# Kernel tuning notes

Measured on AMD Instinct MI355X. Metric: run time of the kernel, lower is better.

The kernel has to match this reference:

```python
import jax, jax.numpy as jnp
import numpy as np

N_NODES = 10000
N_EDGES = 160000
BN_EPS = 1e-5


def _sage(xx, src, dst, Wl, bl, Wr, n):
    # SAGEConv: lin_l(mean of in-neighbors) + lin_r(x)
    s = jax.ops.segment_sum(xx[src], dst, num_segments=n)
    cnt = jax.ops.segment_sum(jnp.ones((src.shape[0], 1), xx.dtype), dst, num_segments=n)
    mean = s / jnp.maximum(cnt, 1.0)
    return mean @ Wl + bl + xx @ Wr


def _gin(xx, src, dst, W1, b1, W2, b2, n):
    # GINConv (eps=0): MLP(x + sum of neighbors), MLP = Lin-ReLU-Lin-ReLU
    agg = xx + jax.ops.segment_sum(xx[src], dst, num_segments=n)
    h = jax.nn.relu(agg @ W1 + b1)
    return jax.nn.relu(h @ W2 + b2)


def _gat(xx, s2, d2, W, a_s, a_d, b, heads, ch, n):
    # GATConv with self-loops already appended in (s2, d2)
    h = (xx @ W).reshape(n, heads, ch)          # [N,H,C]
    al_s = (h * a_s).sum(-1)                     # [N,H]
    al_d = (h * a_d).sum(-1)                     # [N,H]
    e = jax.nn.leaky_relu(al_s[s2] + al_d[d2], negative_slope=0.2)  # [E',H]
    m = jax.ops.segment_max(e, d2, num_segments=n)
    ex = jnp.exp(e - m[d2])
    den = jax.ops.segment_sum(ex, d2, num_segments=n)
    coef = ex / den[d2]                          # segment softmax over dst
    out = jax.ops.segment_sum(h[s2] * coef[:, :, None], d2, num_segments=n)
    return out.reshape(n, heads * ch) + b


def reference(x, edge_index, train_edge_id,
              Wp1, bp1, Wp2, bp2, Wp3, bp3,
              sage1_Wl, sage1_bl, sage1_Wr, sage2_Wl, sage2_bl, sage2_Wr,
              gin1_W1, gin1_b1, gin1_W2, gin1_b2,
              gin2_W1, gin2_b1, gin2_W2, gin2_b2, gin_lin_W, gin_lin_b,
              gat1_W, gat1_as, gat1_ad, gat1_b,
              gat2_W, gat2_as, gat2_ad, gat2_b,
              fusion_w, lin1_W, lin1_b, lin2_W, lin2_b, fc2_W, fc2_b):
    n = x.shape[0]
    src, dst = edge_index[0], edge_index[1]
    # --- ppc: PointNet-style encoder: per-point MLP (16->64->128->256) + max pool over points ---
    pts = x[:, :, :16]                            # [N,L,16]
    h = jax.nn.relu(pts @ Wp1 + bp1)
    h = jax.nn.relu(h @ Wp2 + bp2)
    h = jax.nn.relu(h @ Wp3 + bp3)
    feat = h.max(axis=1)                          # [N,256]
    # --- SAGE branch ---
    hs = jax.nn.relu(_sage(feat, src, dst, sage1_Wl, sage1_bl, sage1_Wr, n))
    out_sage = _sage(hs, src, dst, sage2_Wl, sage2_bl, sage2_Wr, n)
    # --- GIN branch ---
    hg = jax.nn.relu(_gin(feat, src, dst, gin1_W1, gin1_b1, gin1_W2, gin1_b2, n))
    hg = jax.nn.relu(_gin(hg, src, dst, gin2_W1, gin2_b1, gin2_W2, gin2_b2, n))
    out_gin = hg @ gin_lin_W + gin_lin_b
    # --- GAT branch (self-loops per PyG default) ---
    loop = jnp.arange(n)
    s2 = jnp.concatenate([src, loop])
    d2 = jnp.concatenate([dst, loop])
    ha = jax.nn.relu(_gat(feat, s2, d2, gat1_W, gat1_as, gat1_ad, gat1_b, 8, 10, n))
    out_gat = _gat(ha, s2, d2, gat2_W, gat2_as, gat2_ad, gat2_b, 1, 512, n)
    # --- weighted fusion + batch norm (batch stats, no affine) ---
    y = fusion_w[0] * out_sage + fusion_w[1] * out_gin + fusion_w[2] * out_gat
    mu = y.mean(axis=0)
    var = y.var(axis=0)
    y = (y - mu) / jnp.sqrt(var + BN_EPS)
    # --- head ---
    y = jax.nn.relu(y @ lin1_W + lin1_b)
    y = y @ lin2_W + lin2_b
    # --- edge-pair gather + multiply for link scoring ---
    nid = edge_index[:, train_edge_id]            # [2,T]
    z = y[nid[0]] * y[nid[1]]
    return z @ fc2_W + fc2_b                      # [T,7]


def setup_inputs() -> dict:
    key = jax.random.key(0)
    ks = iter(jax.random.split(key, 64))
    def nrm(shape, s=0.02):
        return jax.random.normal(next(ks), shape, dtype=jnp.float32) * s
    inp = {}
    inp['x'] = jax.random.normal(next(ks), (N_NODES, 128, 16), dtype=jnp.float32)
    inp['edge_index'] = jax.random.randint(next(ks), (2, N_EDGES), 0, N_NODES, dtype=jnp.int32)
    inp['train_edge_id'] = jax.random.randint(next(ks), (50000,), 0, N_EDGES, dtype=jnp.int32)
    # ppc point encoder
    inp['Wp1'] = nrm((16, 64)); inp['bp1'] = nrm((64,))
    inp['Wp2'] = nrm((64, 128)); inp['bp2'] = nrm((128,))
    inp['Wp3'] = nrm((128, 256)); inp['bp3'] = nrm((256,))
    # SAGE: 256->128->512
    inp['sage1_Wl'] = nrm((256, 128)); inp['sage1_bl'] = nrm((128,)); inp['sage1_Wr'] = nrm((256, 128))
    inp['sage2_Wl'] = nrm((128, 512)); inp['sage2_bl'] = nrm((512,)); inp['sage2_Wr'] = nrm((128, 512))
    # GIN: 2 convs (256->128->128, 128->128->128) + lin 128->512
    inp['gin1_W1'] = nrm((256, 128)); inp['gin1_b1'] = nrm((128,))
    inp['gin1_W2'] = nrm((128, 128)); inp['gin1_b2'] = nrm((128,))
    inp['gin2_W1'] = nrm((128, 128)); inp['gin2_b1'] = nrm((128,))
    inp['gin2_W2'] = nrm((128, 128)); inp['gin2_b2'] = nrm((128,))
    inp['gin_lin_W'] = nrm((128, 512)); inp['gin_lin_b'] = nrm((512,))
    # GAT: layer1 256 -> 8 heads x 10 (concat=80), layer2 80 -> 512 (1 head)
    inp['gat1_W'] = nrm((256, 80)); inp['gat1_as'] = nrm((8, 10)); inp['gat1_ad'] = nrm((8, 10)); inp['gat1_b'] = nrm((80,))
    inp['gat2_W'] = nrm((80, 512)); inp['gat2_as'] = nrm((1, 512)); inp['gat2_ad'] = nrm((1, 512)); inp['gat2_b'] = nrm((512,))
    # fusion + head
    inp['fusion_w'] = jnp.ones((3,), jnp.float32)
    inp['lin1_W'] = nrm((512, 512)); inp['lin1_b'] = nrm((512,))
    inp['lin2_W'] = nrm((512, 512)); inp['lin2_b'] = nrm((512,))
    inp['fc2_W'] = nrm((512, 7)); inp['fc2_b'] = nrm((7,))
    return inp
```

## Files before the change

### kernel.cpp

```cpp
#include <hip/hip_runtime.h>
#include <math.h>

#define NN 10000
#define NE 160000
#define NT 50000

typedef unsigned short u16;
typedef unsigned int u32;
typedef __attribute__((ext_vector_type(8))) short bf16x8;
typedef __attribute__((ext_vector_type(4))) float f32x4;

__device__ __forceinline__ float bf2f(u16 u) { return __uint_as_float(((u32)u) << 16); }
__device__ __forceinline__ u16 f2bf(float f) {
    u32 x = __float_as_uint(f);
    return (u16)((x + 0x7fffu + ((x >> 16) & 1u)) >> 16);
}
__device__ __forceinline__ u32 cvtpk(float a, float b) {
    u32 r;
    asm("v_cvt_pk_bf16_f32 %0, %1, %2" : "=v"(r) : "v"(a), "v"(b));
    return r;
}
__device__ __forceinline__ float lrelu(float x) { return x > 0.f ? x : 0.2f * x; }

#define MFMA16(a, b, c) __builtin_amdgcn_mfma_f32_16x16x32_bf16((a), (b), (c), 0, 0, 0)

__global__ void k_wfrag(const float* __restrict__ W1, const float* __restrict__ W2,
                        const float* __restrict__ W3,
                        u16* __restrict__ W1f, u16* __restrict__ W2f, u16* __restrict__ W3f) {
    int i = blockIdx.x * 256 + threadIdx.x;
    if (i < 2048) {
        int e = i & 7, l = (i >> 3) & 63, nt = i >> 9;
        int k = (l >> 4) * 8 + e, c = nt * 16 + (l & 15);
        W1f[i] = (k < 16) ? f2bf(W1[k * 64 + c]) : (u16)0;
    }
    if (i < 8192) {
        int e = i & 7, l = (i >> 3) & 63, nt = (i >> 9) & 7, ks = i >> 12;
        int k = ks * 32 + (l >> 4) * 8 + e, c = nt * 16 + (l & 15);
        W2f[i] = f2bf(W2[k * 128 + c]);
    }
    if (i < 32768) {
        int e = i & 7, l = (i >> 3) & 63, nt = (i >> 9) & 15, ks = i >> 13;
        int k = ks * 32 + (l >> 4) * 8 + e, c = nt * 16 + (l & 15);
        W3f[i] = f2bf(W3[k * 256 + c]);
    }
}

__global__ void k_pack(const float* __restrict__ W, u16* __restrict__ Wf, int K, int Mt) {
    int total = (((K + 63) & ~63) >> 5) * Mt * 512;
    for (int i = blockIdx.x * 256 + threadIdx.x; i < total; i += gridDim.x * 256) {
        int e = i & 7, l = (i >> 3) & 63, mt = (i >> 9) % Mt, kk = i / (Mt << 9);
        int k = (kk << 5) + ((l >> 4) << 3) + e;
        int c = (mt << 4) + (l & 15);
        Wf[i] = (k < K) ? f2bf(W[(size_t)k * (Mt << 4) + c]) : (u16)0;
    }
}

__global__ __launch_bounds__(256) void k_pointnet_mfma(
    const float* __restrict__ x,
    const u16* __restrict__ W1f, const float* __restrict__ b1,
    const u16* __restrict__ W2f, const float* __restrict__ b2,
    const u16* __restrict__ W3f, const float* __restrict__ b3,
    u16* __restrict__ featb)
{
    __shared__ __align__(16) u16 buf[16384];

    const int node = blockIdx.x;
    const int t = threadIdx.x;
    const int w = t >> 6;
    const int l = t & 63;
    const int lr = l & 15;
    const int lg = l >> 4;

    u32 pk1[4][2][2];
    {
        union { u32 q[4]; bf16x8 v; } xb0, xb1;
        xb0.q[0] = xb0.q[1] = xb0.q[2] = xb0.q[3] = 0;
        xb1 = xb0;
        if (lg < 2) {
            const float* px = x + ((size_t)node * 128 + w * 32 + lr) * 16 + lg * 8;
            float4 f0 = *(const float4*)px;
            float4 f1 = *(const float4*)(px + 4);
            xb0.q[0] = cvtpk(f0.x, f0.y); xb0.q[1] = cvtpk(f0.z, f0.w);
            xb0.q[2] = cvtpk(f1.x, f1.y); xb0.q[3] = cvtpk(f1.z, f1.w);
            float4 g0 = *(const float4*)(px + 256);
            float4 g1 = *(const float4*)(px + 260);
            xb1.q[0] = cvtpk(g0.x, g0.y); xb1.q[1] = cvtpk(g0.z, g0.w);
            xb1.q[2] = cvtpk(g1.x, g1.y); xb1.q[3] = cvtpk(g1.z, g1.w);
        }
        #pragma unroll
        for (int cht = 0; cht < 4; ++cht) {
            f32x4 ci = *(const f32x4*)(b1 + cht * 16 + 4 * lg);
            bf16x8 wf = *(const bf16x8*)(W1f + (cht * 64 + l) * 8);
            f32x4 a0 = MFMA16(wf, xb0.v, ci);
            f32x4 a1 = MFMA16(wf, xb1.v, ci);
            pk1[cht][0][0] = cvtpk(fmaxf(a0[0], 0.f), fmaxf(a0[1], 0.f));
            pk1[cht][0][1] = cvtpk(fmaxf(a0[2], 0.f), fmaxf(a0[3], 0.f));
            pk1[cht][1][0] = cvtpk(fmaxf(a1[0], 0.f), fmaxf(a1[1], 0.f));
            pk1[cht][1][1] = cvtpk(fmaxf(a1[2], 0.f), fmaxf(a1[3], 0.f));
        }
    }

    {
        f32x4 acc2[8][2];
        #pragma unroll
        for (int mt = 0; mt < 8; ++mt) {
            f32x4 ci = *(const f32x4*)(b2 + mt * 16 + 4 * lg);
            acc2[mt][0] = ci;
            acc2[mt][1] = ci;
        }
        #pragma unroll
        for (int ks = 0; ks < 2; ++ks) {
            union { u32 q[4]; bf16x8 v; } B2[2];
            #pragma unroll
            for (int ptt = 0; ptt < 2; ++ptt) {
                #pragma unroll
                for (int j = 0; j < 4; ++j) {
                    int s = ((2 * (lg & 1) + (j >> 1)) << 4) + lr;
                    int lo = __shfl((int)pk1[2 * ks][ptt][j & 1], s);
                    int hi = __shfl((int)pk1[2 * ks + 1][ptt][j & 1], s);
                    B2[ptt].q[j] = (u32)((lg >> 1) ? hi : lo);
                }
            }
            #pragma unroll
            for (int mt = 0; mt < 8; ++mt) {
                bf16x8 af = *(const bf16x8*)(W2f + ((ks * 8 + mt) * 64 + l) * 8);
                acc2[mt][0] = MFMA16(af, B2[0].v, acc2[mt][0]);
                acc2[mt][1] = MFMA16(af, B2[1].v, acc2[mt][1]);
            }
        }
        #pragma unroll
        for (int mt = 0; mt < 8; ++mt) {
            #pragma unroll
            for (int ptt = 0; ptt < 2; ++ptt) {
                int pt = w * 32 + ptt * 16 + lr;
                int ch0 = mt * 16 + 4 * lg;
                u32 q0 = cvtpk(fmaxf(acc2[mt][ptt][0], 0.f), fmaxf(acc2[mt][ptt][1], 0.f));
                u32 q1 = cvtpk(fmaxf(acc2[mt][ptt][2], 0.f), fmaxf(acc2[mt][ptt][3], 0.f));
                int idx = (pt * 128 + ch0) ^ ((pt & 15) << 3);
                *(uint2*)&buf[idx] = make_uint2(q0, q1);
            }
        }
    }
    __syncthreads();

    {
        float pmax[4] = {0.f, 0.f, 0.f, 0.f};
        #pragma unroll
        for (int half = 0; half < 2; ++half) {
            f32x4 acc3[4][4];
            #pragma unroll
            for (int nt = 0; nt < 4; ++nt) {
                float bv = b3[w * 64 + nt * 16 + lr];
                f32x4 ci = {bv, bv, bv, bv};
                #pragma unroll
                for (int mt = 0; mt < 4; ++mt) acc3[mt][nt] = ci;
            }
            #pragma unroll
            for (int ks = 0; ks < 4; ++ks) {
                bf16x8 bf_[4];
                #pragma unroll
                for (int nt = 0; nt < 4; ++nt)
                    bf_[nt] = *(const bf16x8*)(W3f + ((ks * 16 + w * 4 + nt) * 64 + l) * 8);
                #pragma unroll
                for (int mt = 0; mt < 4; ++mt) {
                    int row = half * 64 + mt * 16 + lr;
                    int elem = row * 128 + ks * 32 + lg * 8;
                    bf16x8 af = *(const bf16x8*)&buf[elem ^ ((row & 15) << 3)];
                    #pragma unroll
                    for (int nt = 0; nt < 4; ++nt)
                        acc3[mt][nt] = MFMA16(af, bf_[nt], acc3[mt][nt]);
                }
            }
            #pragma unroll
            for (int nt = 0; nt < 4; ++nt) {
                #pragma unroll
                for (int mt = 0; mt < 4; ++mt) {
                    pmax[nt] = fmaxf(fmaxf(pmax[nt], acc3[mt][nt][0]),
                                     fmaxf(acc3[mt][nt][1],
                                           fmaxf(acc3[mt][nt][2], acc3[mt][nt][3])));
                }
            }
        }
        #pragma unroll
        for (int nt = 0; nt < 4; ++nt) {
            pmax[nt] = fmaxf(pmax[nt], __shfl_xor(pmax[nt], 16));
            pmax[nt] = fmaxf(pmax[nt], __shfl_xor(pmax[nt], 32));
        }
        if (l < 16) {
            #pragma unroll
            for (int nt = 0; nt < 4; ++nt)
                featb[(size_t)node * 256 + w * 64 + nt * 16 + l] = f2bf(pmax[nt]);
        }
    }
}

template<int CT, int DUAL, int RELU, int OUTM, int NORMA>
__global__ __launch_bounds__(256) void k_mm(
    const u16* __restrict__ A, const u16* __restrict__ A2,
    const u16* __restrict__ Bf, const u16* __restrict__ B2f,
    const float* __restrict__ bias, int K, int Mt,
    void* __restrict__ outp,
    const float* __restrict__ scale_ptr, int scale_idx,
    const float* __restrict__ mu, const float* __restrict__ inv)
{
    __shared__ u16 As[8192];
    __shared__ u16 As2[DUAL ? 8192 : 8];

    const int t = threadIdx.x;
    const int l = t & 63, lr = l & 15, lg = l >> 4;
    const int row0 = blockIdx.y << 7;
    const int ct0 = blockIdx.x * CT;
    const int m0 = (t >> 6) << 5;

    f32x4 acc[2][CT];
    #pragma unroll
    for (int nt = 0; nt < CT; ++nt) {
        float bv = bias ? bias[((ct0 + nt) << 4) + lr] : 0.f;
        f32x4 ci = {bv, bv, bv, bv};
        acc[0][nt] = ci;
        acc[1][nt] = ci;
    }

    const int KS = (K + 63) >> 6;
    for (int kblk = 0; kblk < KS; ++kblk) {
        const int k0 = kblk << 6;
        if (kblk) __syncthreads();
        #pragma unroll
        for (int j = 0; j < 4; ++j) {
            int si = t + (j << 8);
            int row = si >> 3, seg = si & 7;
            int gr = row0 + row;
            int kb = k0 + (seg << 3);
            int soff = ((row << 6) + (seg << 3)) ^ ((row & 7) << 3);
            if (NORMA) {
                u32 q0 = 0, q1 = 0, q2 = 0, q3 = 0;
                if (gr < NN) {
                    const float* Af = (const float*)A;
                    float4 f0 = *(const float4*)(Af + (size_t)gr * K + kb);
                    float4 f1 = *(const float4*)(Af + (size_t)gr * K + kb + 4);
                    q0 = cvtpk((f0.x - mu[kb+0]) * inv[kb+0], (f0.y - mu[kb+1]) * inv[kb+1]);
                    q1 = cvtpk((f0.z - mu[kb+2]) * inv[kb+2], (f0.w - mu[kb+3]) * inv[kb+3]);
                    q2 = cvtpk((f1.x - mu[kb+4]) * inv[kb+4], (f1.y - mu[kb+5]) * inv[kb+5]);
                    q3 = cvtpk((f1.z - mu[kb+6]) * inv[kb+6], (f1.w - mu[kb+7]) * inv[kb+7]);
                }
                u32* dst = (u32*)&As[soff];
                dst[0] = q0; dst[1] = q1; dst[2] = q2; dst[3] = q3;
            } else {
                bf16x8 v = {0,0,0,0,0,0,0,0};
                bf16x8 v2 = {0,0,0,0,0,0,0,0};
                if (gr < NN) {
                    if (kb + 8 <= K) {
                        v = *(const bf16x8*)(A + (size_t)gr * K + kb);
                        if (DUAL) v2 = *(const bf16x8*)(A2 + (size_t)gr * K + kb);
                    } else {
                        #pragma unroll
                        for (int e = 0; e < 8; ++e) if (kb + e < K) {
                            v[e] = (short)A[(size_t)gr * K + kb + e];
                            if (DUAL) v2[e] = (short)A2[(size_t)gr * K + kb + e];
                        }
                    }
                }
                *(bf16x8*)&As[soff] = v;
                if (DUAL) *(bf16x8*)&As2[soff] = v2;
            }
        }
        __syncthreads();
        #pragma unroll
        for (int ks = 0; ks < 2; ++ks) {
            const int kk = (k0 >> 5) + ks;
            bf16x8 bfr[CT];
            #pragma unroll
            for (int nt = 0; nt < CT; ++nt)
                bfr[nt] = *(const bf16x8*)(Bf + (((size_t)kk * Mt + ct0 + nt) << 9) + (l << 3));
            #pragma unroll
            for (int mt = 0; mt < 2; ++mt) {
                int row = m0 + (mt << 4) + lr;
                int soff = ((row << 6) + (ks << 5) + (lg << 3)) ^ ((row & 7) << 3);
                bf16x8 af = *(const bf16x8*)&As[soff];
                #pragma unroll
                for (int nt = 0; nt < CT; ++nt)
                    acc[mt][nt] = MFMA16(af, bfr[nt], acc[mt][nt]);
            }
            if (DUAL) {
                bf16x8 bfr2[CT];
                #pragma unroll
                for (int nt = 0; nt < CT; ++nt)
                    bfr2[nt] = *(const bf16x8*)(B2f + (((size_t)kk * Mt + ct0 + nt) << 9) + (l << 3));
                #pragma unroll
                for (int mt = 0; mt < 2; ++mt) {
                    int row = m0 + (mt << 4) + lr;
                    int soff = ((row << 6) + (ks << 5) + (lg << 3)) ^ ((row & 7) << 3);
                    bf16x8 af2 = *(const bf16x8*)&As2[soff];
                    #pragma unroll
                    for (int nt = 0; nt < CT; ++nt)
                        acc[mt][nt] = MFMA16(af2, bfr2[nt], acc[mt][nt]);
                }
            }
        }
    }

    float scale = 1.f;
    if (OUTM == 1 || OUTM == 2) scale = scale_ptr[scale_idx];
    const int M = Mt << 4;
    #pragma unroll
    for (int mt = 0; mt < 2; ++mt) {
        #pragma unroll
        for (int nt = 0; nt < CT; ++nt) {
            int col = ((ct0 + nt) << 4) + lr;
            #pragma unroll
            for (int r = 0; r < 4; ++r) {
                int grow = row0 + m0 + (mt << 4) + (lg << 2) + r;
                if (grow >= NN) continue;
                float v = acc[mt][nt][r];
                if (RELU) v = fmaxf(v, 0.f);
                size_t o = (size_t)grow * M + col;
                if (OUTM == 0) ((u16*)outp)[o] = f2bf(v);
                else if (OUTM == 1) ((float*)outp)[o] = scale * v;
                else if (OUTM == 2) ((float*)outp)[o] += scale * v;
                else ((float*)outp)[o] = v;
            }
        }
    }
}

__global__ void k_init(int* counts, float* s1, float* s2) {
    int i = blockIdx.x * 256 + threadIdx.x;
    if (i < NN) counts[i] = 0;
    if (i < 512) { s1[i] = 0.f; s2[i] = 0.f; }
}

__global__ void k_csr_count(const int* __restrict__ EI, int* counts) {
    int e = blockIdx.x * 256 + threadIdx.x;
    if (e < NE) atomicAdd(&counts[EI[NE + e]], 1);
}

__global__ __launch_bounds__(1024) void k_scan(const int* __restrict__ counts,
                                               int* offs, int* cursor) {
    __shared__ int buf[1024];
    int t = threadIdx.x;
    int carry = 0;
    for (int chunk = 0; chunk < (NN + 1023) / 1024; ++chunk) {
        int i = chunk * 1024 + t;
        int v = (i < NN) ? counts[i] : 0;
        buf[t] = v;
        __syncthreads();
        for (int o = 1; o < 1024; o <<= 1) {
            int xv = (t >= o) ? buf[t - o] : 0;
            __syncthreads();
            buf[t] += xv;
            __syncthreads();
        }
        int excl = buf[t] - v;
        if (i < NN) { offs[i] = carry + excl; cursor[i] = carry + excl; }
        carry += buf[1023];
        __syncthreads();
    }
    if (t == 0) offs[NN] = carry;
}

__global__ void k_csr_scatter(const int* __restrict__ EI, int* cursor, int* csrc) {
    int e = blockIdx.x * 256 + threadIdx.x;
    if (e < NE) {
        int d = EI[NE + e];
        int pos = atomicAdd(&cursor[d], 1);
        csrc[pos] = EI[e];
    }
}

template<int WU>
__global__ void k_agg2same(const u32* __restrict__ in, u32* __restrict__ out_mean,
                           u32* __restrict__ out_agg,
                           const int* __restrict__ offs, const int* __restrict__ srcs)
{
    int node = blockIdx.x;
    int c = threadIdx.x;
    int o0 = offs[node], o1 = offs[node + 1];
    float s0 = 0.f, s1 = 0.f;
    for (int j = o0; j < o1; ++j) {
        u32 v = in[(size_t)srcs[j] * WU + c];
        s0 += bf2f((u16)(v & 0xffff));
        s1 += bf2f((u16)(v >> 16));
    }
    int d = o1 - o0;
    float r = 1.f / (float)(d > 0 ? d : 1);
    out_mean[(size_t)node * WU + c] = cvtpk(s0 * r, s1 * r);
    u32 v = in[(size_t)node * WU + c];
    out_agg[(size_t)node * WU + c] = cvtpk(s0 + bf2f((u16)(v & 0xffff)),
                                           s1 + bf2f((u16)(v >> 16)));
}

template<int WU>
__global__ void k_agg2two(const u32* __restrict__ inM, const u32* __restrict__ inS,
                          u32* __restrict__ outM, u32* __restrict__ outS,
                          const int* __restrict__ offs, const int* __restrict__ srcs)
{
    int node = blockIdx.x;
    int c = threadIdx.x;
    int o0 = offs[node], o1 = offs[node + 1];
    float m0 = 0.f, m1 = 0.f, s0 = 0.f, s1 = 0.f;
    for (int j = o0; j < o1; ++j) {
        int sc = srcs[j];
        u32 a = inM[(size_t)sc * WU + c];
        u32 b = inS[(size_t)sc * WU + c];
        m0 += bf2f((u16)(a & 0xffff)); m1 += bf2f((u16)(a >> 16));
        s0 += bf2f((u16)(b & 0xffff)); s1 += bf2f((u16)(b >> 16));
    }
    int d = o1 - o0;
    float r = 1.f / (float)(d > 0 ? d : 1);
    outM[(size_t)node * WU + c] = cvtpk(m0 * r, m1 * r);
    u32 v = inS[(size_t)node * WU + c];
    outS[(size_t)node * WU + c] = cvtpk(s0 + bf2f((u16)(v & 0xffff)),
                                        s1 + bf2f((u16)(v >> 16)));
}

__global__ void k_gat1_al(const u16* __restrict__ h, const float* __restrict__ a_s,
                          const float* __restrict__ a_d, float* als, float* ald) {
    int idx = blockIdx.x * 64 + threadIdx.x;
    if (idx >= NN * 8) return;
    int node = idx >> 3, hh = idx & 7;
    float s = 0.f, d = 0.f;
    #pragma unroll
    for (int c = 0; c < 10; ++c) {
        float hv = bf2f(h[node * 80 + hh * 10 + c]);
        s = fmaf(hv, a_s[hh * 10 + c], s);
        d = fmaf(hv, a_d[hh * 10 + c], d);
    }
    als[idx] = s; ald[idx] = d;
}

__global__ __launch_bounds__(128) void k_gat1_attn(
    const u16* __restrict__ h, const float* __restrict__ als,
    const float* __restrict__ ald, const float* __restrict__ bias,
    const int* __restrict__ offs, const int* __restrict__ srcs,
    u16* __restrict__ ha)
{
    int node = blockIdx.x;
    int t = threadIdx.x;
    if (t >= 80) return;
    int hh = t / 10;
    int o0 = offs[node], o1 = offs[node + 1];
    float ad = ald[node * 8 + hh];
    float eself = lrelu(als[node * 8 + hh] + ad);
    float m = eself;
    for (int j = o0; j < o1; ++j)
        m = fmaxf(m, lrelu(als[srcs[j] * 8 + hh] + ad));
    float den = 0.f, num = 0.f;
    {
        float wgt = __expf(eself - m);
        den += wgt; num += wgt * bf2f(h[(size_t)node * 80 + t]);
    }
    for (int j = o0; j < o1; ++j) {
        int sc = srcs[j];
        float wgt = __expf(lrelu(als[sc * 8 + hh] + ad) - m);
        den += wgt; num += wgt * bf2f(h[(size_t)sc * 80 + t]);
    }
    ha[(size_t)node * 80 + t] = f2bf(fmaxf(num / den + bias[t], 0.f));
}

__global__ __launch_bounds__(256) void k_gat2_al(
    const u16* __restrict__ h, const float* __restrict__ a_s,
    const float* __restrict__ a_d, float* als, float* ald)
{
    __shared__ float rs[256], rd[256];
    int node = blockIdx.x, t = threadIdx.x;
    float h0 = bf2f(h[(size_t)node * 512 + t]);
    float h1 = bf2f(h[(size_t)node * 512 + 256 + t]);
    rs[t] = h0 * a_s[t] + h1 * a_s[256 + t];
    rd[t] = h0 * a_d[t] + h1 * a_d[256 + t];
    __syncthreads();
    for (int o = 128; o > 0; o >>= 1) {
        if (t < o) { rs[t] += rs[t + o]; rd[t] += rd[t + o]; }
        __syncthreads();
    }
    if (t == 0) { als[node] = rs[0]; ald[node] = rd[0]; }
}

__global__ __launch_bounds__(256) void k_gat2_attn(
    const u16* __restrict__ h, const float* __restrict__ als,
    const float* __restrict__ ald, const float* __restrict__ bias,
    const int* __restrict__ offs, const int* __restrict__ srcs,
    const float* __restrict__ fusion_w, float* __restrict__ Y)
{
    int node = blockIdx.x;
    int t = threadIdx.x;
    float w2 = fusion_w[2];
    int o0 = offs[node], o1 = offs[node + 1];
    float ad = ald[node];
    float eself = lrelu(als[node] + ad);
    float m = eself;
    for (int j = o0; j < o1; ++j) m = fmaxf(m, lrelu(als[srcs[j]] + ad));
    float den = 0.f, n0 = 0.f, n1 = 0.f;
    {
        float wgt = __expf(eself - m);
        den += wgt;
        n0 += wgt * bf2f(h[(size_t)node * 512 + t]);
        n1 += wgt * bf2f(h[(size_t)node * 512 + 256 + t]);
    }
    for (int j = o0; j < o1; ++j) {
        int sc = srcs[j];
        float wgt = __expf(lrelu(als[sc] + ad) - m);
        den += wgt;
        n0 += wgt * bf2f(h[(size_t)sc * 512 + t]);
        n1 += wgt * bf2f(h[(size_t)sc * 512 + 256 + t]);
    }
    Y[(size_t)node * 512 + t]       += w2 * (n0 / den + bias[t]);
    Y[(size_t)node * 512 + 256 + t] += w2 * (n1 / den + bias[256 + t]);
}

__global__ __launch_bounds__(256) void k_bn_stats(const float* __restrict__ Y,
                                                  float* ssum, float* ssq) {
    int t = threadIdx.x;
    int b = blockIdx.x;
    int r0 = b * 40, r1 = r0 + 40;
    if (r1 > NN) r1 = NN;
    float s0 = 0, s1 = 0, q0 = 0, q1 = 0;
    for (int r = r0; r < r1; ++r) {
        float v0 = Y[(size_t)r * 512 + t];
        float v1 = Y[(size_t)r * 512 + 256 + t];
        s0 += v0; q0 += v0 * v0; s1 += v1; q1 += v1 * v1;
    }
    atomicAdd(&ssum[t], s0); atomicAdd(&ssum[256 + t], s1);
    atomicAdd(&ssq[t], q0);  atomicAdd(&ssq[256 + t], q1);
}

__global__ void k_bn_final(const float* ssum, const float* ssq, float* mu, float* inv) {
    int c = blockIdx.x * 256 + threadIdx.x;
    if (c < 512) {
        float m = ssum[c] / (float)NN;
        float v = ssq[c] / (float)NN - m * m;
        mu[c] = m;
        inv[c] = rsqrtf(v + 1e-5f);
    }
}

__global__ __launch_bounds__(256) void k_final(
    const float* __restrict__ y2, const int* __restrict__ EI,
    const int* __restrict__ tid, const float* __restrict__ fcW,
    const float* __restrict__ fcb, float* __restrict__ out)
{
    int pair = blockIdx.x * 4 + (threadIdx.x >> 6);
    int lane = threadIdx.x & 63;
    if (pair >= NT) return;
    int eid = tid[pair];
    int a = EI[eid], b = EI[NE + eid];
    float acc[7] = {};
    for (int c = lane; c < 512; c += 64) {
        float v = y2[(size_t)a * 512 + c] * y2[(size_t)b * 512 + c];
        #pragma unroll
        for (int j = 0; j < 7; ++j) acc[j] = fmaf(v, fcW[c * 7 + j], acc[j]);
    }
    for (int o = 32; o > 0; o >>= 1) {
        #pragma unroll
        for (int j = 0; j < 7; ++j) acc[j] += __shfl_down(acc[j], o);
    }
    if (lane == 0) {
        #pragma unroll
        for (int j = 0; j < 7; ++j) out[(size_t)pair * 7 + j] = acc[j] + fcb[j];
    }
}

extern "C" void kernel_launch(void* const* d_in, const int* in_sizes, int n_in,
                              void* d_out, int out_size, void* d_ws, size_t ws_size,
                              hipStream_t stream)
{
    (void)in_sizes; (void)n_in; (void)out_size; (void)ws_size;
    const float* x        = (const float*)d_in[0];
    const int*   EI       = (const int*)d_in[1];
    const int*   tid      = (const int*)d_in[2];
    const float* Wp1      = (const float*)d_in[3];
    const float* bp1      = (const float*)d_in[4];
    const float* Wp2      = (const float*)d_in[5];
    const float* bp2      = (const float*)d_in[6];
    const float* Wp3      = (const float*)d_in[7];
    const float* bp3      = (const float*)d_in[8];
    const float* sage1_Wl = (const float*)d_in[9];
    const float* sage1_bl = (const float*)d_in[10];
    const float* sage1_Wr = (const float*)d_in[11];
    const float* sage2_Wl = (const float*)d_in[12];
    const float* sage2_bl = (const float*)d_in[13];
    const float* sage2_Wr = (const float*)d_in[14];
    const float* gin1_W1  = (const float*)d_in[15];
    const float* gin1_b1  = (const float*)d_in[16];
    const float* gin1_W2  = (const float*)d_in[17];
    const float* gin1_b2  = (const float*)d_in[18];
    const float* gin2_W1  = (const float*)d_in[19];
    const float* gin2_b1  = (const float*)d_in[20];
    const float* gin2_W2  = (const float*)d_in[21];
    const float* gin2_b2  = (const float*)d_in[22];
    const float* gin_lin_W= (const float*)d_in[23];
    const float* gin_lin_b= (const float*)d_in[24];
    const float* gat1_W   = (const float*)d_in[25];
    const float* gat1_as  = (const float*)d_in[26];
    const float* gat1_ad  = (const float*)d_in[27];
    const float* gat1_b   = (const float*)d_in[28];
    const float* gat2_W   = (const float*)d_in[29];
    const float* gat2_as  = (const float*)d_in[30];
    const float* gat2_ad  = (const float*)d_in[31];
    const float* gat2_b   = (const float*)d_in[32];
    const float* fusion_w = (const float*)d_in[33];
    const float* lin1_W   = (const float*)d_in[34];
    const float* lin1_b   = (const float*)d_in[35];
    const float* lin2_W   = (const float*)d_in[36];
    const float* lin2_b   = (const float*)d_in[37];
    const float* fc2_W    = (const float*)d_in[38];
    const float* fc2_b    = (const float*)d_in[39];

    char* base = (char*)d_ws;
    u16* mean1 = (u16*)base;
    u16* agg1  = (u16*)(base + 5120000);
    u16* h2b   = (u16*)base;
    u16* y1b   = (u16*)(base + 20480000);
    float* y2  = (float*)base;
    size_t off = 40960000;
    u16* featb = (u16*)(base + off); off += 5120000;
    u16* hsb   = (u16*)(base + off); off += 2560000;
    u16* mean2 = (u16*)(base + off); off += 2560000;
    u16* g1    = (u16*)(base + off); off += 2560000;
    u16* g2    = (u16*)(base + off); off += 2560000;
    u16* hgat  = (u16*)(base + off); off += 1600000;
    u16* hab   = (u16*)(base + off); off += 1600000;
    float* Y   = (float*)(base + off); off += 20480000;
    float* als1 = (float*)(base + off); off += 320000;
    float* ald1 = (float*)(base + off); off += 320000;
    float* als2 = (float*)(base + off); off += 40000;
    float* ald2 = (float*)(base + off); off += 40000;
    float* ssum = (float*)(base + off); off += 2048;
    float* ssq  = (float*)(base + off); off += 2048;
    float* mu   = (float*)(base + off); off += 2048;
    float* inv  = (float*)(base + off); off += 2048;
    int* counts = (int*)(base + off); off += 40000;
    int* offs   = (int*)(base + off); off += 40016;
    int* cursor = (int*)(base + off); off += 40000;
    int* csrc   = (int*)(base + off); off += 640000;
    u16* W1f    = (u16*)(base + off); off += 4096;
    u16* W2f    = (u16*)(base + off); off += 16384;
    u16* W3f    = (u16*)(base + off); off += 65536;
    u16* s1lf   = (u16*)(base + off); off += 65536;
    u16* s1rf   = (u16*)(base + off); off += 65536;
    u16* g1w1f  = (u16*)(base + off); off += 65536;
    u16* g1w2f  = (u16*)(base + off); off += 32768;
    u16* ga1f   = (u16*)(base + off); off += 40960;
    u16* s2lf   = (u16*)(base + off); off += 131072;
    u16* s2rf   = (u16*)(base + off); off += 131072;
    u16* g2w1f  = (u16*)(base + off); off += 32768;
    u16* g2w2f  = (u16*)(base + off); off += 32768;
    u16* glinf  = (u16*)(base + off); off += 131072;
    u16* ga2f   = (u16*)(base + off); off += 131072;
    u16* l1f    = (u16*)(base + off); off += 524288;
    u16* l2f    = (u16*)(base + off); off += 524288;

    k_init<<<40, 256, 0, stream>>>(counts, ssum, ssq);
    k_wfrag<<<128, 256, 0, stream>>>(Wp1, Wp2, Wp3, W1f, W2f, W3f);
    k_pack<<<256, 256, 0, stream>>>(sage1_Wl, s1lf, 256, 8);
    k_pack<<<256, 256, 0, stream>>>(sage1_Wr, s1rf, 256, 8);
    k_pack<<<256, 256, 0, stream>>>(gin1_W1,  g1w1f, 256, 8);
    k_pack<<<256, 256, 0, stream>>>(gin1_W2,  g1w2f, 128, 8);
    k_pack<<<256, 256, 0, stream>>>(gat1_W,   ga1f, 256, 5);
    k_pack<<<256, 256, 0, stream>>>(sage2_Wl, s2lf, 128, 32);
    k_pack<<<256, 256, 0, stream>>>(sage2_Wr, s2rf, 128, 32);
    k_pack<<<256, 256, 0, stream>>>(gin2_W1,  g2w1f, 128, 8);
    k_pack<<<256, 256, 0, stream>>>(gin2_W2,  g2w2f, 128, 8);
    k_pack<<<256, 256, 0, stream>>>(gin_lin_W, glinf, 128, 32);
    k_pack<<<256, 256, 0, stream>>>(gat2_W,   ga2f, 80, 32);
    k_pack<<<256, 256, 0, stream>>>(lin1_W,   l1f, 512, 32);
    k_pack<<<256, 256, 0, stream>>>(lin2_W,   l2f, 512, 32);

    k_pointnet_mfma<<<NN, 256, 0, stream>>>(x, W1f, bp1, W2f, bp2, W3f, bp3, featb);
    k_csr_count<<<(NE + 255) / 256, 256, 0, stream>>>(EI, counts);
    k_scan<<<1, 1024, 0, stream>>>(counts, offs, cursor);
    k_csr_scatter<<<(NE + 255) / 256, 256, 0, stream>>>(EI, cursor, csrc);

    dim3 gN128(4, 79), gN80(5, 79), gWide(4, 79);

    k_agg2same<128><<<NN, 128, 0, stream>>>((const u32*)featb, (u32*)mean1, (u32*)agg1,
                                            offs, csrc);

    k_mm<2,1,1,0,0><<<gN128, 256, 0, stream>>>(mean1, featb, s1lf, s1rf, sage1_bl,
                                               256, 8, hsb, nullptr, 0, nullptr, nullptr);
    k_mm<2,0,1,0,0><<<gN128, 256, 0, stream>>>(agg1, nullptr, g1w1f, nullptr, gin1_b1,
                                               256, 8, g1, nullptr, 0, nullptr, nullptr);
    k_mm<2,0,1,0,0><<<gN128, 256, 0, stream>>>(g1, nullptr, g1w2f, nullptr, gin1_b2,
                                               128, 8, g2, nullptr, 0, nullptr, nullptr);

    k_agg2two<64><<<NN, 64, 0, stream>>>((const u32*)hsb, (const u32*)g2,
                                         (u32*)mean2, (u32*)g1, offs, csrc);

    k_mm<1,0,0,0,0><<<gN80, 256, 0, stream>>>(featb, nullptr, ga1f, nullptr, nullptr,
                                              256, 5, hgat, nullptr, 0, nullptr, nullptr);
    k_gat1_al<<<1250, 64, 0, stream>>>(hgat, gat1_as, gat1_ad, als1, ald1);
    k_gat1_attn<<<NN, 128, 0, stream>>>(hgat, als1, ald1, gat1_b, offs, csrc, hab);

    k_mm<8,1,0,1,0><<<gWide, 256, 0, stream>>>(mean2, hsb, s2lf, s2rf, sage2_bl,
                                               128, 32, Y, fusion_w, 0, nullptr, nullptr);
    k_mm<2,0,1,0,0><<<gN128, 256, 0, stream>>>(g1, nullptr, g2w1f, nullptr, gin2_b1,
                                               128, 8, g2, nullptr, 0, nullptr, nullptr);
    k_mm<2,0,1,0,0><<<gN128, 256, 0, stream>>>(g2, nullptr, g2w2f, nullptr, gin2_b2,
                                               128, 8, g1, nullptr, 0, nullptr, nullptr);
    k_mm<8,0,0,2,0><<<gWide, 256, 0, stream>>>(g1, nullptr, glinf, nullptr, gin_lin_b,
                                               128, 32, Y, fusion_w, 1, nullptr, nullptr);
    k_mm<8,0,0,0,0><<<gWide, 256, 0, stream>>>(hab, nullptr, ga2f, nullptr, nullptr,
                                               80, 32, h2b, nullptr, 0, nullptr, nullptr);
    k_gat2_al<<<NN, 256, 0, stream>>>(h2b, gat2_as, gat2_ad, als2, ald2);
    k_gat2_attn<<<NN, 256, 0, stream>>>(h2b, als2, ald2, gat2_b, offs, csrc, fusion_w, Y);

    k_bn_stats<<<250, 256, 0, stream>>>(Y, ssum, ssq);
    k_bn_final<<<2, 256, 0, stream>>>(ssum, ssq, mu, inv);
    k_mm<8,0,1,0,1><<<gWide, 256, 0, stream>>>((const u16*)Y, nullptr, l1f, nullptr, lin1_b,
                                               512, 32, y1b, nullptr, 0, mu, inv);
    k_mm<8,0,0,3,0><<<gWide, 256, 0, stream>>>(y1b, nullptr, l2f, nullptr, lin2_b,
                                               512, 32, y2, nullptr, 0, nullptr, nullptr);

    k_final<<<(NT + 3) / 4, 256, 0, stream>>>(y2, EI, tid, fc2_W, fc2_b, (float*)d_out);
}
```

Before: 564.6 us.

## Keep PointNet layer-2 activations in registers and store lin2 output as bf16

The PointNet kernel no longer stages the 128x128 layer-2 activations in shared memory. It reshuffles the packed bf16 results across lanes with shuffles and feeds them directly as MFMA operands for layer 3. Each wave now covers all 256 output channels for its own 32 points and max-pools with lane shuffles plus a small cross-wave shared reduction. This removes the big LDS buffer and the LDS round trip, at the cost of more register pressure and more weight reads per wave. Separately, the lin2 output is written in bf16 instead of fp32, halving the traffic into the final edge gather at some precision cost.

```diff
diff --git a/kernel.cpp b/kernel.cpp
--- a/kernel.cpp
+++ b/kernel.cpp
@@ -62,7 +62,7 @@
     const u16* __restrict__ W3f, const float* __restrict__ b3,
     u16* __restrict__ featb)
 {
-    __shared__ __align__(16) u16 buf[16384];
+    __shared__ float pool[4][256];
 
     const int node = blockIdx.x;
     const int t = threadIdx.x;
@@ -100,6 +100,7 @@
         }
     }
 
+    u32 pk2[8][2][2];
     {
         f32x4 acc2[8][2];
         #pragma unroll
@@ -132,65 +133,65 @@
         for (int mt = 0; mt < 8; ++mt) {
             #pragma unroll
             for (int ptt = 0; ptt < 2; ++ptt) {
-                int pt = w * 32 + ptt * 16 + lr;
-                int ch0 = mt * 16 + 4 * lg;
-                u32 q0 = cvtpk(fmaxf(acc2[mt][ptt][0], 0.f), fmaxf(acc2[mt][ptt][1], 0.f));
-                u32 q1 = cvtpk(fmaxf(acc2[mt][ptt][2], 0.f), fmaxf(acc2[mt][ptt][3], 0.f));
-                int idx = (pt * 128 + ch0) ^ ((pt & 15) << 3);
-                *(uint2*)&buf[idx] = make_uint2(q0, q1);
-            }
+                pk2[mt][ptt][0] = cvtpk(fmaxf(acc2[mt][ptt][0], 0.f), fmaxf(acc2[mt][ptt][1], 0.f));
+                pk2[mt][ptt][1] = cvtpk(fmaxf(acc2[mt][ptt][2], 0.f), fmaxf(acc2[mt][ptt][3], 0.f));
+            }
+        }
+    }
+
+    union { u32 q[4]; bf16x8 v; } B3[4][2];
+    #pragma unroll
+    for (int ks = 0; ks < 4; ++ks) {
+        #pragma unroll
+        for (int ptt = 0; ptt < 2; ++ptt) {
+            #pragma unroll
+            for (int j = 0; j < 4; ++j) {
+                int s = ((2 * (lg & 1) + (j >> 1)) << 4) + lr;
+                int lo = __shfl((int)pk2[2 * ks][ptt][j & 1], s);
+                int hi = __shfl((int)pk2[2 * ks + 1][ptt][j & 1], s);
+                B3[ks][ptt].q[j] = (u32)((lg >> 1) ? hi : lo);
+            }
+        }
+    }
+
+    #pragma unroll
+    for (int half = 0; half < 2; ++half) {
+        f32x4 acc3[8][2];
+        #pragma unroll
+        for (int oc = 0; oc < 8; ++oc) {
+            f32x4 ci = *(const f32x4*)(b3 + (half * 8 + oc) * 16 + 4 * lg);
+            acc3[oc][0] = ci;
+            acc3[oc][1] = ci;
+        }
+        #pragma unroll
+        for (int ks = 0; ks < 4; ++ks) {
+            #pragma unroll
+            for (int oc = 0; oc < 8; ++oc) {
+                bf16x8 af = *(const bf16x8*)(W3f + ((ks * 16 + half * 8 + oc) * 64 + l) * 8);
+                acc3[oc][0] = MFMA16(af, B3[ks][0].v, acc3[oc][0]);
+                acc3[oc][1] = MFMA16(af, B3[ks][1].v, acc3[oc][1]);
+            }
+        }
+        #pragma unroll
+        for (int oc = 0; oc < 8; ++oc) {
+            f32x4 m;
+            #pragma unroll
+            for (int r = 0; r < 4; ++r)
+                m[r] = fmaxf(fmaxf(acc3[oc][0][r], acc3[oc][1][r]), 0.f);
+            #pragma unroll
+            for (int o = 1; o < 16; o <<= 1) {
+                #pragma unroll
+                for (int r = 0; r < 4; ++r)
+                    m[r] = fmaxf(m[r], __shfl_xor(m[r], o));
+            }
+            if (lr == 0)
+                *(f32x4*)&pool[w][(half * 8 + oc) * 16 + 4 * lg] = m;
         }
     }
     __syncthreads();
-
-    {
-        float pmax[4] = {0.f, 0.f, 0.f, 0.f};
-        #pragma unroll
-        for (int half = 0; half < 2; ++half) {
-            f32x4 acc3[4][4];
-            #pragma unroll
-            for (int nt = 0; nt < 4; ++nt) {
-                float bv = b3[w * 64 + nt * 16 + lr];
-                f32x4 ci = {bv, bv, bv, bv};
-                #pragma unroll
-                for (int mt = 0; mt < 4; ++mt) acc3[mt][nt] = ci;
-            }
-            #pragma unroll
-            for (int ks = 0; ks < 4; ++ks) {
-                bf16x8 bf_[4];
-                #pragma unroll
-                for (int nt = 0; nt < 4; ++nt)
-                    bf_[nt] = *(const bf16x8*)(W3f + ((ks * 16 + w * 4 + nt) * 64 + l) * 8);
-                #pragma unroll
-                for (int mt = 0; mt < 4; ++mt) {
-                    int row = half * 64 + mt * 16 + lr;
-                    int elem = row * 128 + ks * 32 + lg * 8;
-                    bf16x8 af = *(const bf16x8*)&buf[elem ^ ((row & 15) << 3)];
-                    #pragma unroll
-                    for (int nt = 0; nt < 4; ++nt)
-                        acc3[mt][nt] = MFMA16(af, bf_[nt], acc3[mt][nt]);
-                }
-            }
-            #pragma unroll
-            for (int nt = 0; nt < 4; ++nt) {
-                #pragma unroll
-                for (int mt = 0; mt < 4; ++mt) {
-                    pmax[nt] = fmaxf(fmaxf(pmax[nt], acc3[mt][nt][0]),
-                                     fmaxf(acc3[mt][nt][1],
-                                           fmaxf(acc3[mt][nt][2], acc3[mt][nt][3])));
-                }
-            }
-        }
-        #pragma unroll
-        for (int nt = 0; nt < 4; ++nt) {
-            pmax[nt] = fmaxf(pmax[nt], __shfl_xor(pmax[nt], 16));
-            pmax[nt] = fmaxf(pmax[nt], __shfl_xor(pmax[nt], 32));
-        }
-        if (l < 16) {
-            #pragma unroll
-            for (int nt = 0; nt < 4; ++nt)
-                featb[(size_t)node * 256 + w * 64 + nt * 16 + l] = f2bf(pmax[nt]);
-        }
+    if (t < 256) {
+        float v = fmaxf(fmaxf(pool[0][t], pool[1][t]), fmaxf(pool[2][t], pool[3][t]));
+        featb[(size_t)node * 256 + t] = f2bf(v);
     }
 }
 
@@ -534,7 +535,7 @@
 }
 
 __global__ __launch_bounds__(256) void k_final(
-    const float* __restrict__ y2, const int* __restrict__ EI,
+    const u16* __restrict__ y2, const int* __restrict__ EI,
     const int* __restrict__ tid, const float* __restrict__ fcW,
     const float* __restrict__ fcb, float* __restrict__ out)
 {
@@ -545,7 +546,7 @@
     int a = EI[eid], b = EI[NE + eid];
     float acc[7] = {};
     for (int c = lane; c < 512; c += 64) {
-        float v = y2[(size_t)a * 512 + c] * y2[(size_t)b * 512 + c];
+        float v = bf2f(y2[(size_t)a * 512 + c]) * bf2f(y2[(size_t)b * 512 + c]);
         #pragma unroll
         for (int j = 0; j < 7; ++j) acc[j] = fmaf(v, fcW[c * 7 + j], acc[j]);
     }
@@ -610,7 +611,7 @@
     u16* agg1  = (u16*)(base + 5120000);
     u16* h2b   = (u16*)base;
     u16* y1b   = (u16*)(base + 20480000);
-    float* y2  = (float*)base;
+    u16* y2b   = (u16*)base;
     size_t off = 40960000;
     u16* featb = (u16*)(base + off); off += 5120000;
     u16* hsb   = (u16*)(base + off); off += 2560000;
@@ -707,8 +708,8 @@
     k_bn_final<<<2, 256, 0, stream>>>(ssum, ssq, mu, inv);
     k_mm<8,0,1,0,1><<<gWide, 256, 0, stream>>>((const u16*)Y, nullptr, l1f, nullptr, lin1_b,
                                                512, 32, y1b, nullptr, 0, mu, inv);
-    k_mm<8,0,0,3,0><<<gWide, 256, 0, stream>>>(y1b, nullptr, l2f, nullptr, lin2_b,
-                                               512, 32, y2, nullptr, 0, nullptr, nullptr);
-
-    k_final<<<(NT + 3) / 4, 256, 0, stream>>>(y2, EI, tid, fc2_W, fc2_b, (float*)d_out);
-}
+    k_mm<8,0,0,0,0><<<gWide, 256, 0, stream>>>(y1b, nullptr, l2f, nullptr, lin2_b,
+                                               512, 32, y2b, nullptr, 0, nullptr, nullptr);
+
+    k_final<<<(NT + 3) / 4, 256, 0, stream>>>(y2b, EI, tid, fc2_W, fc2_b, (float*)d_out);
+}
```

New measurement: 670.9 us. +18.8%, slower.
